# Kernel tuning notes

Measured on AMD Instinct MI355X. Metric: run time of the kernel, lower is better.

## Reference

```python
import jax, jax.numpy as jnp
import numpy as np
from jax import lax

B, NMEAS, M, LAYER_NUM = 2048, 128, 256, 10
CLAMP_MIN, CLAMP_MAX = 1e-6, 100.0
EPS_S = 1e-6


def _conv2d(x, w, b):
    y = lax.conv_general_dilated(x, w, (1, 1), 'SAME', dimension_numbers=('NCHW', 'OIHW', 'NCHW'))
    return y + b[None, :, None, None]


def _conv1d(x, w, b):
    y = lax.conv_general_dilated(x, w, (1,), 'SAME', dimension_numbers=('NCH', 'OIH', 'NCH'))
    return y + b[None, :, None]


def setup_inputs():
    key = jax.random.key(0)
    ks = jax.random.split(key, 12)
    s = 1.0 / np.sqrt(2.0 * NMEAS)  # ~unit-norm dictionary columns
    return {
        'Yr': jax.random.normal(ks[0], (B, 1, NMEAS, 1), jnp.float32),
        'Yi': jax.random.normal(ks[1], (B, 1, NMEAS, 1), jnp.float32),
        'Ar': s * jax.random.normal(ks[2], (NMEAS, M), jnp.float32),
        'Ai': s * jax.random.normal(ks[3], (NMEAS, M), jnp.float32),
        'conv1_w': 0.1 * jax.random.normal(ks[4], (32, 2, 3, 3), jnp.float32),
        'conv1_b': jnp.zeros((32,), jnp.float32),
        'conv2_w': 0.1 * jax.random.normal(ks[5], (64, 32, 3, 3), jnp.float32),
        'conv2_b': jnp.zeros((64,), jnp.float32),
        'hc_w': 0.1 * jax.random.normal(ks[6], (LAYER_NUM - 1, 64, 3), jnp.float32),
        'hc_b': jnp.zeros((LAYER_NUM - 1,), jnp.float32),
        'hd_w': 0.1 * jax.random.normal(ks[7], (LAYER_NUM - 1, 64, 3), jnp.float32),
        'hd_b': jnp.zeros((LAYER_NUM - 1,), jnp.float32),
        'hT_w': 0.1 * jax.random.normal(ks[8], (LAYER_NUM, 64, 3), jnp.float32),
        'hT_b': jnp.zeros((LAYER_NUM,), jnp.float32),
        'a0': jnp.asarray(1.0, jnp.float32),
        'b0': jnp.asarray(1.0, jnp.float32),
    }


def _hypernet(ay, c1w, c1b, c2w, c2b, hcw, hcb, hdw, hdb, hTw, hTb):
    # ay: [B, 2, M]; batch acts as image width (context)
    x_img = jnp.transpose(ay, (1, 2, 0))[None]              # [1, 2, M, B]
    f = jax.nn.relu(_conv2d(x_img, c1w, c1b))               # [1, 32, M, B]
    f = jax.nn.relu(_conv2d(f, c2w, c2b))                   # [1, 64, M, B]
    f = jnp.mean(f, axis=2)                                 # AdaptiveAvgPool2d((1,None)) -> [1, 64, B]
    c = jnp.abs(_conv1d(f, hcw, hcb))[0].T                  # [B, L-1]
    d = jnp.abs(_conv1d(f, hdw, hdb))[0].T                  # [B, L-1]
    T = jnp.abs(_conv1d(f, hTw, hTb))[0].T                  # [B, L]
    c = jnp.clip(c, CLAMP_MIN, CLAMP_MAX)
    d = jnp.maximum(d, CLAMP_MIN)
    T = jnp.clip(T, CLAMP_MIN, CLAMP_MAX)
    return c, d, T


def _forward(Yr, Yi, Ar, Ai, conv1_w, conv1_b, conv2_w, conv2_b,
             hc_w, hc_b, hd_w, hd_b, hT_w, hT_b, a0, b0):
    Y = (Yr + 1j * Yi).astype(jnp.complex64)                # [B,1,Nmeas,1]
    A = (Ar + 1j * Ai).astype(jnp.complex64)                # [Nmeas,M]
    AT = A.conj().T                                         # [M,Nmeas]
    AA = AT @ A                                             # [M,M] Hermitian
    AY = jnp.matmul(AT, Y)                                  # [B,1,M,1]
    b = Y.shape[0]
    n = Y.shape[2]
    ay = jnp.concatenate([AY.real.reshape(b, 1, -1), AY.imag.reshape(b, 1, -1)], axis=1)  # [B,2,M]
    c, d, T = _hypernet(ay, conv1_w, conv1_b, conv2_w, conv2_b,
                        hc_w, hc_b, hd_w, hd_b, hT_w, hT_b)
    D = jnp.real(jnp.diagonal(AA))[None, None, :, None]     # diag of Hermitian AA is real; [1,1,M,1]
    eps = (a0 / b0).astype(jnp.complex64) * jnp.ones((b, 1, 1, 1), jnp.complex64)
    Lam = ((c[:, 0] / d[:, 0])[:, None, None, None] * jnp.ones((1, 1, M, 1), jnp.float32)).astype(jnp.complex64)
    U = jnp.zeros((b, 1, M, 1), jnp.complex64)
    a = a0 + n
    for k in range(LAYER_NUM - 1):
        Tk = T[:, k][:, None, None, None]
        # fused SBL/VAMP mean update
        U = eps * (Tk * U - jnp.matmul(AA, U) + AY) / (eps * Tk + Lam + EPS_S)
        Sigma = 1.0 / (eps * D + Lam + EPS_S)
        r = Y - jnp.matmul(A, U)
        eps1 = jnp.sum(r.real ** 2 + r.imag ** 2, axis=(2, 3), keepdims=True)  # ||.||_F^2
        eps2 = jnp.sum(D * Sigma, axis=(2, 3), keepdims=True)
        eps = a / (b0 + eps1 + eps2 + EPS_S)
        Lam = (c[:, k][:, None, None, None] + 1.0) / (
            d[:, k][:, None, None, None] + jnp.abs(U) ** 2 + Sigma + EPS_S)
    Tk = T[:, LAYER_NUM - 1][:, None, None, None]
    U = eps * (Tk * U - jnp.matmul(AA, U) + AY) / (eps * Tk + Lam + EPS_S)
    Ua = jnp.abs(U)
    Ua = Ua / (jnp.max(Ua) + 1e-8)
    return Ua, c, d, T


def reference(Yr, Yi, Ar, Ai, conv1_w, conv1_b, conv2_w, conv2_b,
              hc_w, hc_b, hd_w, hd_b, hT_w, hT_b, a0, b0):
    Ua, c, d, T = _forward(Yr, Yi, Ar, Ai, conv1_w, conv1_b, conv2_w, conv2_b,
                           hc_w, hc_b, hd_w, hd_b, hT_w, hT_b, a0, b0)
    # original returns the last batch row of c/d/T (detached diagnostics)
    return Ua, c[-1:, :], d[-1:, :], T[-1:, :]
```

## Files before the change

### kernel.cpp

```cpp
#include <hip/hip_runtime.h>
#include <math.h>

#define B_N   2048
#define NM    128
#define M_N   256
#define LNUM  10
#define EPS_Sf 1e-6f

typedef _Float16 half8 __attribute__((ext_vector_type(8)));
typedef float floatx4 __attribute__((ext_vector_type(4)));

__device__ __forceinline__ float frcp(float x) { return __builtin_amdgcn_rcpf(x); }

static constexpr size_t o_AA  = 0;
static constexpr size_t o_D   = o_AA  + 131072;
static constexpr size_t o_yn  = o_D   + 256;
static constexpr size_t o_AY  = o_yn  + 2048;
static constexpr size_t o_AYt = o_AY  + 1048576;
static constexpr size_t o_w2t = o_AYt + 1048576;
static constexpr size_t o_z1  = o_w2t + 18432;
static constexpr size_t o_fp  = o_z1  + 16777216;
static constexpr size_t o_f   = o_fp  + 2097152;
static constexpr size_t o_c   = o_f   + 131072;
static constexpr size_t o_dd  = o_c   + 18432;
static constexpr size_t o_T   = o_dd  + 18432;
static constexpr size_t o_Ua  = o_T   + 20480;
static constexpr size_t o_gm  = o_Ua  + 524288;

#define Z1T_RS (2050 * 32)

__global__ void k_pre(const float* __restrict__ Ar, const float* __restrict__ Ai,
                      const float* __restrict__ Yr, const float* __restrict__ Yi,
                      const float* __restrict__ w2, float* __restrict__ ws) {
    __shared__ float sb[2048];
    int blk = blockIdx.x;
    int tid = threadIdx.x;
    if (blk < 256) {
        float* cr = sb; float* ci = sb + NM;
        int i = blk, j = tid;
        if (j < NM) { cr[j] = Ar[j * M_N + i]; ci[j] = Ai[j * M_N + i]; }
        __syncthreads();
        float sr = 0.f, si = 0.f;
        for (int n = 0; n < NM; ++n) {
            float ar = Ar[n * M_N + j], ai = Ai[n * M_N + j];
            sr += cr[n] * ar + ci[n] * ai;
            si += cr[n] * ai - ci[n] * ar;
        }
        _Float16* A16 = (_Float16*)(ws + o_AA);
        size_t off = ((size_t)((i >> 4) * 8 + (j >> 5)) * 64
                      + (size_t)(((j >> 3) & 3) * 16 + (i & 15))) * 8 + (j & 7);
        A16[off]         = (_Float16)sr;
        A16[65536 + off] = (_Float16)si;
        if (j == i) ws[o_D + i] = sr;
        if (i == 0 && j == 0) *(unsigned int*)(ws + o_gm) = 0u;
    } else if (blk < 328) {
        int i = (blk - 256) * 256 + tid;
        if (i < 64 * 32 * 9) {
            int oc = i / 288, r = i % 288;
            int ic = r / 9, kk = r % 9;
            _Float16* Wa = (_Float16*)(ws + o_w2t);
            Wa[((size_t)oc * 9 + kk) * 32 + ic] = (_Float16)w2[i];
        }
    } else {
        float2* Ys = (float2*)sb;
        int bb0 = (blk - 328) * 8;
        for (int i = tid; i < 8 * NM; i += 256) {
            int g = i >> 7, n = i & 127;
            Ys[g * NM + n] = make_float2(Yr[(size_t)(bb0 + g) * NM + n],
                                         Yi[(size_t)(bb0 + g) * NM + n]);
        }
        __syncthreads();
        if (tid < 8) {
            float s = 0.f;
            for (int n = 0; n < NM; ++n) { float2 y = Ys[tid * NM + n]; s += y.x * y.x + y.y * y.y; }
            ws[o_yn + bb0 + tid] = s;
        }
        int m = tid;
        float accr[8], acci[8];
#pragma unroll
        for (int g = 0; g < 8; ++g) { accr[g] = 0.f; acci[g] = 0.f; }
        for (int n = 0; n < NM; ++n) {
            float ar = Ar[n * M_N + m], ai = Ai[n * M_N + m];
#pragma unroll
            for (int g = 0; g < 8; ++g) {
                float2 y = Ys[g * NM + n];
                accr[g] += ar * y.x + ai * y.y;
                acci[g] += ar * y.y - ai * y.x;
            }
        }
        float2* AY = (float2*)(ws + o_AY);
#pragma unroll
        for (int g = 0; g < 8; ++g) {
            AY[(size_t)(bb0 + g) * M_N + m] = make_float2(accr[g], acci[g]);
            ws[o_AYt + (size_t)m * B_N + (bb0 + g)] = accr[g];
            ws[o_AYt + 524288 + (size_t)m * B_N + (bb0 + g)] = acci[g];
        }
    }
}

__global__ void k_conv1(const float* __restrict__ w1, const float* __restrict__ b1,
                        float* __restrict__ ws) {
    __shared__ float w1s[576], b1s[32];
    int tid = threadIdx.x;
    for (int i = tid; i < 576; i += 256) w1s[i] = w1[i];
    if (tid < 32) b1s[tid] = b1[tid];
    __syncthreads();
    int gidx = blockIdx.x * 256 + tid;
    int b = gidx & (B_N - 1), m = gidx >> 11;
    const float* xr = ws + o_AYt;
    float x[2][3][3];
#pragma unroll
    for (int c = 0; c < 2; ++c)
#pragma unroll
        for (int dm = 0; dm < 3; ++dm) {
            int mm = m + dm - 1;
#pragma unroll
            for (int db = 0; db < 3; ++db) {
                int bb = b + db - 1;
                x[c][dm][db] = (mm >= 0 && mm < M_N && bb >= 0 && bb < B_N)
                                 ? xr[(size_t)c * 524288 + (size_t)mm * B_N + bb] : 0.f;
            }
        }
    _Float16* z1t = (_Float16*)(ws + o_z1);
    _Float16 zv[32];
    for (int oc = 0; oc < 32; ++oc) {
        float acc = b1s[oc];
#pragma unroll
        for (int c = 0; c < 2; ++c)
#pragma unroll
            for (int dm = 0; dm < 3; ++dm)
#pragma unroll
                for (int db = 0; db < 3; ++db)
                    acc += x[c][dm][db] * w1s[oc * 18 + c * 9 + dm * 3 + db];
        zv[oc] = (_Float16)fmaxf(acc, 0.f);
    }
    _Float16* dst = z1t + (size_t)(m + 1) * Z1T_RS + (size_t)(b + 1) * 32;
#pragma unroll
    for (int v = 0; v < 4; ++v) *(half8*)(dst + v * 8) = *(half8*)(zv + v * 8);
    half8 z8 = (half8)((_Float16)0.f);
    if (m == 0) {
        _Float16* d2 = z1t + (size_t)(b + 1) * 32;
#pragma unroll
        for (int v = 0; v < 4; ++v) *(half8*)(d2 + v * 8) = z8;
        if (b == 0) { _Float16* d3 = z1t;
#pragma unroll
            for (int v = 0; v < 4; ++v) *(half8*)(d3 + v * 8) = z8; }
        if (b == B_N - 1) { _Float16* d3 = z1t + (size_t)2049 * 32;
#pragma unroll
            for (int v = 0; v < 4; ++v) *(half8*)(d3 + v * 8) = z8; }
    }
    if (m == M_N - 1) {
        _Float16* d2 = z1t + (size_t)257 * Z1T_RS + (size_t)(b + 1) * 32;
#pragma unroll
        for (int v = 0; v < 4; ++v) *(half8*)(d2 + v * 8) = z8;
        if (b == 0) { _Float16* d3 = z1t + (size_t)257 * Z1T_RS;
#pragma unroll
            for (int v = 0; v < 4; ++v) *(half8*)(d3 + v * 8) = z8; }
        if (b == B_N - 1) { _Float16* d3 = z1t + (size_t)257 * Z1T_RS + (size_t)2049 * 32;
#pragma unroll
            for (int v = 0; v < 4; ++v) *(half8*)(d3 + v * 8) = z8; }
    }
    if (b == 0) {
        _Float16* d2 = z1t + (size_t)(m + 1) * Z1T_RS;
#pragma unroll
        for (int v = 0; v < 4; ++v) *(half8*)(d2 + v * 8) = z8;
    }
    if (b == B_N - 1) {
        _Float16* d2 = z1t + (size_t)(m + 1) * Z1T_RS + (size_t)2049 * 32;
#pragma unroll
        for (int v = 0; v < 4; ++v) *(half8*)(d2 + v * 8) = z8;
    }
}

#define MFMA16(A,Bv,C) C = __builtin_amdgcn_mfma_f32_16x16x32_f16(A, Bv, C, 0, 0, 0)
__global__ void __launch_bounds__(128)
k_conv2m(const float* __restrict__ b2, float* __restrict__ ws) {
    int tid = threadIdx.x;
    int lane = tid & 63, wv = tid >> 6;
    int col = lane & 15, quad = lane >> 4;
    int bt = blockIdx.x & 127, g = blockIdx.x >> 7;
    int b0 = bt * 16, m0 = g * 16;
    int oc0w = wv * 32;
    const _Float16* z1t = (const _Float16*)(ws + o_z1);
    const _Float16* Wa  = (const _Float16*)(ws + o_w2t);

    half8 Af[2][9];
#pragma unroll
    for (int t = 0; t < 2; ++t)
#pragma unroll
        for (int kk = 0; kk < 9; ++kk)
            Af[t][kk] = *(const half8*)(Wa + ((size_t)(oc0w + t * 16 + col) * 9 + kk) * 32 + quad * 8);
    float bias[2][4];
#pragma unroll
    for (int t = 0; t < 2; ++t)
#pragma unroll
        for (int r = 0; r < 4; ++r)
            bias[t][r] = b2[oc0w + t * 16 + quad * 4 + r];

    const _Float16* zb = z1t + (size_t)(b0 + col) * 32 + quad * 8;
    half8 Bf[3][3];
#pragma unroll
    for (int ph = 0; ph < 3; ++ph)
#pragma unroll
        for (int db = 0; db < 3; ++db)
            Bf[ph][db] = *(const half8*)(zb + (size_t)(m0 + ph) * Z1T_RS + (size_t)db * 32);

    floatx4 facc[2];
    facc[0] = (floatx4){0.f, 0.f, 0.f, 0.f};
    facc[1] = (floatx4){0.f, 0.f, 0.f, 0.f};

#pragma unroll
    for (int mm = 0; mm < 16; ++mm) {
        floatx4 a0 = (floatx4){0.f, 0.f, 0.f, 0.f};
        floatx4 a1 = (floatx4){0.f, 0.f, 0.f, 0.f};
#pragma unroll
        for (int dm = 0; dm < 3; ++dm) {
            int ph = (mm + dm) % 3;
#pragma unroll
            for (int db = 0; db < 3; ++db) {
                MFMA16(Af[0][dm * 3 + db], Bf[ph][db], a0);
                MFMA16(Af[1][dm * 3 + db], Bf[ph][db], a1);
            }
        }
#pragma unroll
        for (int r = 0; r < 4; ++r) {
            facc[0][r] += fmaxf(a0[r] + bias[0][r], 0.f);
            facc[1][r] += fmaxf(a1[r] + bias[1][r], 0.f);
        }
        if (mm < 15) {
            int ph = mm % 3;
#pragma unroll
            for (int db = 0; db < 3; ++db)
                Bf[ph][db] = *(const half8*)(zb + (size_t)(m0 + mm + 3) * Z1T_RS + (size_t)db * 32);
        }
    }
    float* fp = ws + o_fp + (size_t)g * 131072;
#pragma unroll
    for (int t = 0; t < 2; ++t)
#pragma unroll
        for (int r = 0; r < 4; ++r)
            fp[(size_t)(oc0w + t * 16 + quad * 4 + r) * B_N + b0 + col] = facc[t][r];
}

__global__ void k_fred(float* __restrict__ ws) {
    size_t i = (size_t)blockIdx.x * 256 + threadIdx.x;
    float s = 0.f;
    for (int p = 0; p < 16; ++p) s += ws[o_fp + (size_t)p * 131072 + i];
    ws[o_f + i] = s * (1.f / 256.f);
}

__global__ void k_cdt(const float* __restrict__ hcw, const float* __restrict__ hcb,
                      const float* __restrict__ hdw, const float* __restrict__ hdb,
                      const float* __restrict__ hTw, const float* __restrict__ hTb,
                      float* __restrict__ ws, float* __restrict__ out) {
    int l = blockIdx.x >> 3;
    int b = (blockIdx.x & 7) * 256 + threadIdx.x;
    const float* f = ws + o_f;
    const float* w; float bi; int li, kind;
    if (l < 9)       { kind = 0; li = l;      w = hcw + (size_t)li * 192; bi = hcb[li]; }
    else if (l < 18) { kind = 1; li = l - 9;  w = hdw + (size_t)li * 192; bi = hdb[li]; }
    else             { kind = 2; li = l - 18; w = hTw + (size_t)li * 192; bi = hTb[li]; }
    __shared__ float wsm[192];
    for (int i = threadIdx.x; i < 192; i += 256) wsm[i] = w[i];
    __syncthreads();
    float acc = bi;
    bool okL = (b > 0), okR = (b < B_N - 1);
    for (int ic = 0; ic < 64; ++ic) {
        const float* fr = f + (size_t)ic * B_N + b;
        float fm1 = okL ? fr[-1] : 0.f;
        float f0  = fr[0];
        float fp1 = okR ? fr[1] : 0.f;
        acc += fm1 * wsm[ic * 3] + f0 * wsm[ic * 3 + 1] + fp1 * wsm[ic * 3 + 2];
    }
    float v = fmaxf(fabsf(acc), 1e-6f);
    if (kind != 1) v = fminf(v, 100.f);
    if (kind == 0)      { ws[o_c  + (size_t)b * 9  + li] = v; if (b == B_N - 1) out[524288 + li] = v; }
    else if (kind == 1) { ws[o_dd + (size_t)b * 9  + li] = v; if (b == B_N - 1) out[524297 + li] = v; }
    else                { ws[o_T  + (size_t)b * 10 + li] = v; if (b == B_N - 1) out[524306 + li] = v; }
}

__global__ void __launch_bounds__(1024, 4)
k_iter(const float* __restrict__ a0p, const float* __restrict__ b0p, float* __restrict__ ws) {
    __shared__ __align__(16) _Float16 Ubf[2][8][64][8];
    __shared__ __align__(16) float redv[16][52];
    __shared__ float redm[16];
    int tid = threadIdx.x;
    int lane = tid & 63, w = tid >> 6;
    int col = lane & 15, quad = lane >> 4;
    int b = blockIdx.x * 16 + col;
    const float2* AY = (const float2*)(ws + o_AY);
    const _Float16* Af = (const _Float16*)(ws + o_AA);
    float a0 = a0p[0], b0v = b0p[0];
    float atot = a0 + (float)NM;
    float yn = ws[o_yn + b];
    float eps = a0 / b0v;
    float Tv[10], cv[9], dvv[9];
#pragma unroll
    for (int i = 0; i < 10; ++i) Tv[i] = ws[o_T + (size_t)b * 10 + i];
#pragma unroll
    for (int i = 0; i < 9; ++i) cv[i] = ws[o_c + (size_t)b * 9 + i];
#pragma unroll
    for (int i = 0; i < 9; ++i) dvv[i] = ws[o_dd + (size_t)b * 9 + i];
    float lam0 = cv[0] * frcp(dvv[0]);
    half8 Ar8[8], Ai8[8];
#pragma unroll
    for (int ks = 0; ks < 8; ++ks) {
        const _Float16* ab = Af + ((size_t)(w * 8 + ks) * 64 + lane) * 8;
        Ar8[ks] = *(const half8*)(ab);
        Ai8[ks] = *(const half8*)(ab + 65536);
    }
    float Dv[4], ayr[4], ayi[4], lam[4], Ur[4], Ui[4], sg[4], wr_[4], wi_[4];
#pragma unroll
    for (int r = 0; r < 4; ++r) {
        int m = w * 16 + quad * 4 + r;
        Dv[r] = ws[o_D + m];
        float2 a = AY[(size_t)b * M_N + m];
        ayr[r] = a.x; ayi[r] = a.y;
        lam[r] = lam0;
        Ur[r] = 0.f; Ui[r] = 0.f; wr_[r] = 0.f; wi_[r] = 0.f;
    }
    int ksw = w >> 1;
    int quadD = (w & 1) * 2 + (quad >> 1);
    int laneD = quadD * 16 + col;
    int eb = (quad & 1) * 4;
    for (int k = 0; k < LNUM; ++k) {
        float Tk = Tv[k];
#pragma unroll
        for (int r = 0; r < 4; ++r) {
            float iv = eps * frcp(fmaf(eps, Tk, lam[r] + EPS_Sf));
            Ur[r] = iv * (Tk * Ur[r] - wr_[r] + ayr[r]);
            Ui[r] = iv * (Tk * Ui[r] - wi_[r] + ayi[r]);
        }
        if (k == LNUM - 1) break;
        {
            union { _Float16 h[4]; unsigned long long u; } c0, c2;
#pragma unroll
            for (int r = 0; r < 4; ++r) {
                c0.h[r] = (_Float16)Ur[r];
                c2.h[r] = (_Float16)Ui[r];
            }
            *(unsigned long long*)&Ubf[0][ksw][laneD][eb] = c0.u;
            *(unsigned long long*)&Ubf[1][ksw][laneD][eb] = c2.u;
        }
        __syncthreads();
        floatx4 wrp = (floatx4){0.f, 0.f, 0.f, 0.f};
        floatx4 wrn = (floatx4){0.f, 0.f, 0.f, 0.f};
        floatx4 wia1 = (floatx4){0.f, 0.f, 0.f, 0.f};
        floatx4 wia2 = (floatx4){0.f, 0.f, 0.f, 0.f};
#pragma unroll
        for (int ks = 0; ks < 8; ++ks) {
            half8 urh = *(const half8*)&Ubf[0][ks][lane][0];
            half8 uih = *(const half8*)&Ubf[1][ks][lane][0];
            MFMA16(Ar8[ks], urh, wrp);
            MFMA16(Ai8[ks], uih, wrn);
            MFMA16(Ar8[ks], uih, wia1);
            MFMA16(Ai8[ks], urh, wia2);
        }
        float p1 = 0.f, p2 = 0.f, p3 = 0.f;
#pragma unroll
        for (int r = 0; r < 4; ++r) {
            wr_[r] = wrp[r] - wrn[r];
            wi_[r] = wia1[r] + wia2[r];
            sg[r] = frcp(fmaf(eps, Dv[r], lam[r] + EPS_Sf));
            p1 += ayr[r] * Ur[r] + ayi[r] * Ui[r];
            p2 += Ur[r] * wr_[r] + Ui[r] * wi_[r];
            p3 += Dv[r] * sg[r];
        }
        p1 += __shfl_xor(p1, 16); p1 += __shfl_xor(p1, 32);
        p2 += __shfl_xor(p2, 16); p2 += __shfl_xor(p2, 32);
        p3 += __shfl_xor(p3, 16); p3 += __shfl_xor(p3, 32);
        if (lane < 16) {
            redv[col][w * 3]     = p1;
            redv[col][w * 3 + 1] = p2;
            redv[col][w * 3 + 2] = p3;
        }
        __syncthreads();
        float s[3] = {0.f, 0.f, 0.f};
#pragma unroll
        for (int j = 0; j < 12; ++j) {
            floatx4 v4 = *(const floatx4*)&redv[col][j * 4];
#pragma unroll
            for (int e = 0; e < 4; ++e) s[(j * 4 + e) % 3] += v4[e];
        }
        float eps1 = fmaxf(yn - 2.f * s[0] + s[1], 0.f);
        eps = atot * frcp(b0v + eps1 + s[2] + EPS_Sf);
        float ck1 = cv[k] + 1.f;
        float dk = dvv[k];
#pragma unroll
        for (int r = 0; r < 4; ++r)
            lam[r] = ck1 * frcp(dk + Ur[r] * Ur[r] + Ui[r] * Ui[r] + sg[r] + EPS_Sf);
    }
    float4 v;
    v.x = sqrtf(Ur[0] * Ur[0] + Ui[0] * Ui[0]);
    v.y = sqrtf(Ur[1] * Ur[1] + Ui[1] * Ui[1]);
    v.z = sqrtf(Ur[2] * Ur[2] + Ui[2] * Ui[2]);
    v.w = sqrtf(Ur[3] * Ur[3] + Ui[3] * Ui[3]);
    *(float4*)&ws[o_Ua + (size_t)b * M_N + w * 16 + quad * 4] = v;
    float lm = fmaxf(fmaxf(v.x, v.y), fmaxf(v.z, v.w));
#pragma unroll
    for (int off = 32; off >= 1; off >>= 1) lm = fmaxf(lm, __shfl_xor(lm, off));
    if (lane == 0) redm[w] = lm;
    __syncthreads();
    if (tid == 0) {
        float mx = redm[0];
#pragma unroll
        for (int i = 1; i < 16; ++i) mx = fmaxf(mx, redm[i]);
        atomicMax((unsigned int*)(ws + o_gm), __float_as_uint(mx));
    }
}

__global__ void k_norm(const float* __restrict__ ws, float* __restrict__ out) {
    size_t i = (size_t)blockIdx.x * 256 + threadIdx.x;
    float gm = __uint_as_float(*(const unsigned int*)(ws + o_gm));
    out[i] = ws[o_Ua + i] / (gm + 1e-8f);
}

extern "C" void kernel_launch(void* const* d_in, const int* in_sizes, int n_in,
                              void* d_out, int out_size, void* d_ws, size_t ws_size,
                              hipStream_t stream) {
    (void)in_sizes; (void)n_in; (void)out_size; (void)ws_size;
    const float* Yr  = (const float*)d_in[0];
    const float* Yi  = (const float*)d_in[1];
    const float* Ar  = (const float*)d_in[2];
    const float* Ai  = (const float*)d_in[3];
    const float* w1  = (const float*)d_in[4];
    const float* b1  = (const float*)d_in[5];
    const float* w2  = (const float*)d_in[6];
    const float* b2  = (const float*)d_in[7];
    const float* hcw = (const float*)d_in[8];
    const float* hcb = (const float*)d_in[9];
    const float* hdw = (const float*)d_in[10];
    const float* hdb = (const float*)d_in[11];
    const float* hTw = (const float*)d_in[12];
    const float* hTb = (const float*)d_in[13];
    const float* a0  = (const float*)d_in[14];
    const float* b0  = (const float*)d_in[15];
    float* ws = (float*)d_ws;
    float* out = (float*)d_out;

    k_pre   <<<584, 256, 0, stream>>>(Ar, Ai, Yr, Yi, w2, ws);
    k_conv1 <<<2048, 256, 0, stream>>>(w1, b1, ws);
    k_conv2m<<<2048, 128, 0, stream>>>(b2, ws);
    k_fred  <<<512, 256, 0, stream>>>(ws);
    k_cdt   <<<224, 256, 0, stream>>>(hcw, hcb, hdw, hdb, hTw, hTb, ws, out);
    k_iter  <<<128, 1024, 0, stream>>>(a0, b0, ws);
    k_norm  <<<2048, 256, 0, stream>>>(ws, out);
}
```

Measured before the change: 224.9 us.

## Fuse pooled-feature reduction into conv2 via atomics and drop redundant AY buffer

Removes the k_fred kernel and its 16-way partial-sum buffer. conv2 now atomically adds its scaled partial means straight into the feature array, which extra blocks in k_pre zero first. The interleaved AY write is dropped, and k_iter reads the transposed AYt copy instead. The Ua output goes through shared memory so global stores are contiguous. This saves one launch and some workspace traffic, but adds atomic contention, nondeterministic summation order, and strided AYt reads in k_iter.

```diff
diff --git a/kernel.cpp b/kernel.cpp
--- a/kernel.cpp
+++ b/kernel.cpp
@@ -61,7 +61,7 @@
             _Float16* Wa = (_Float16*)(ws + o_w2t);
             Wa[((size_t)oc * 9 + kk) * 32 + ic] = (_Float16)w2[i];
         }
-    } else {
+    } else if (blk < 584) {
         float2* Ys = (float2*)sb;
         int bb0 = (blk - 328) * 8;
         for (int i = tid; i < 8 * NM; i += 256) {
@@ -88,13 +88,14 @@
                 acci[g] += ar * y.y - ai * y.x;
             }
         }
-        float2* AY = (float2*)(ws + o_AY);
 #pragma unroll
         for (int g = 0; g < 8; ++g) {
-            AY[(size_t)(bb0 + g) * M_N + m] = make_float2(accr[g], acci[g]);
             ws[o_AYt + (size_t)m * B_N + (bb0 + g)] = accr[g];
             ws[o_AYt + 524288 + (size_t)m * B_N + (bb0 + g)] = acci[g];
         }
+    } else {
+        size_t i = (size_t)(blk - 584) * 1024 + tid * 4;
+        *(float4*)&ws[o_f + i] = make_float4(0.f, 0.f, 0.f, 0.f);
     }
 }
 
@@ -234,19 +235,13 @@
                 Bf[ph][db] = *(const half8*)(zb + (size_t)(m0 + mm + 3) * Z1T_RS + (size_t)db * 32);
         }
     }
-    float* fp = ws + o_fp + (size_t)g * 131072;
+    float* f = ws + o_f;
 #pragma unroll
     for (int t = 0; t < 2; ++t)
 #pragma unroll
         for (int r = 0; r < 4; ++r)
-            fp[(size_t)(oc0w + t * 16 + quad * 4 + r) * B_N + b0 + col] = facc[t][r];
-}
-
-__global__ void k_fred(float* __restrict__ ws) {
-    size_t i = (size_t)blockIdx.x * 256 + threadIdx.x;
-    float s = 0.f;
-    for (int p = 0; p < 16; ++p) s += ws[o_fp + (size_t)p * 131072 + i];
-    ws[o_f + i] = s * (1.f / 256.f);
+            atomicAdd(&f[(size_t)(oc0w + t * 16 + quad * 4 + r) * B_N + b0 + col],
+                      facc[t][r] * (1.f / 256.f));
 }
 
 __global__ void k_cdt(const float* __restrict__ hcw, const float* __restrict__ hcb,
@@ -283,12 +278,12 @@
 k_iter(const float* __restrict__ a0p, const float* __restrict__ b0p, float* __restrict__ ws) {
     __shared__ __align__(16) _Float16 Ubf[2][8][64][8];
     __shared__ __align__(16) float redv[16][52];
+    __shared__ __align__(16) float UaT[16][260];
     __shared__ float redm[16];
     int tid = threadIdx.x;
     int lane = tid & 63, w = tid >> 6;
     int col = lane & 15, quad = lane >> 4;
     int b = blockIdx.x * 16 + col;
-    const float2* AY = (const float2*)(ws + o_AY);
     const _Float16* Af = (const _Float16*)(ws + o_AA);
     float a0 = a0p[0], b0v = b0p[0];
     float atot = a0 + (float)NM;
@@ -314,8 +309,8 @@
     for (int r = 0; r < 4; ++r) {
         int m = w * 16 + quad * 4 + r;
         Dv[r] = ws[o_D + m];
-        float2 a = AY[(size_t)b * M_N + m];
-        ayr[r] = a.x; ayi[r] = a.y;
+        ayr[r] = ws[o_AYt + (size_t)m * B_N + b];
+        ayi[r] = ws[o_AYt + 524288 + (size_t)m * B_N + b];
         lam[r] = lam0;
         Ur[r] = 0.f; Ui[r] = 0.f; wr_[r] = 0.f; wi_[r] = 0.f;
     }
@@ -395,8 +390,11 @@
     v.y = sqrtf(Ur[1] * Ur[1] + Ui[1] * Ui[1]);
     v.z = sqrtf(Ur[2] * Ur[2] + Ui[2] * Ui[2]);
     v.w = sqrtf(Ur[3] * Ur[3] + Ui[3] * Ui[3]);
-    *(float4*)&ws[o_Ua + (size_t)b * M_N + w * 16 + quad * 4] = v;
-    float lm = fmaxf(fmaxf(v.x, v.y), fmaxf(v.z, v.w));
+    *(float4*)&UaT[col][w * 16 + quad * 4] = v;
+    __syncthreads();
+    float4 v2 = *(const float4*)&UaT[w][lane * 4];
+    *(float4*)&ws[o_Ua + (size_t)(blockIdx.x * 16 + w) * M_N + lane * 4] = v2;
+    float lm = fmaxf(fmaxf(v2.x, v2.y), fmaxf(v2.z, v2.w));
 #pragma unroll
     for (int off = 32; off >= 1; off >>= 1) lm = fmaxf(lm, __shfl_xor(lm, off));
     if (lane == 0) redm[w] = lm;
@@ -438,10 +436,9 @@
     float* ws = (float*)d_ws;
     float* out = (float*)d_out;
 
-    k_pre   <<<584, 256, 0, stream>>>(Ar, Ai, Yr, Yi, w2, ws);
+    k_pre   <<<712, 256, 0, stream>>>(Ar, Ai, Yr, Yi, w2, ws);
     k_conv1 <<<2048, 256, 0, stream>>>(w1, b1, ws);
     k_conv2m<<<2048, 128, 0, stream>>>(b2, ws);
-    k_fred  <<<512, 256, 0, stream>>>(ws);
     k_cdt   <<<224, 256, 0, stream>>>(hcw, hcb, hdw, hdb, hTw, hTb, ws, out);
     k_iter  <<<128, 1024, 0, stream>>>(a0, b0, ws);
     k_norm  <<<2048, 256, 0, stream>>>(ws, out);
```

After: 233.0 us. +3.6%, slower.
